# Kernel tuning notes

Measured on AMD Instinct MI355X. Metric: run time of the kernel, lower is better.

## Reference

```python
import jax, jax.numpy as jnp
import numpy as np

B, L, TQ, D, H, S = 4, 64, 8, 768, 12, 2000
E = D // H
EPS = 1e-5


def _ln(x, g, b):
    m = jnp.mean(x, axis=-1, keepdims=True)
    v = jnp.mean(jnp.square(x - m), axis=-1, keepdims=True)
    return (x - m) * jax.lax.rsqrt(v + EPS) * g + b


def setup_inputs() -> dict:
    key = jax.random.key(0)
    ks = jax.random.split(key, 8)
    w = 0.02
    return {
        "target_tokens": jax.random.normal(ks[0], (B, L, TQ, D), jnp.float32),
        "key_bank": jax.random.normal(ks[1], (S, D), jnp.float32),
        "value_bank": jax.random.normal(ks[2], (S, D), jnp.float32),
        "bank_mask": jnp.ones((S,), jnp.int32),
        "Wq": jax.random.normal(ks[3], (D, D), jnp.float32) * w,
        "bq": jnp.zeros((D,), jnp.float32),
        "Wk": jax.random.normal(ks[4], (D, D), jnp.float32) * w,
        "bk": jnp.zeros((D,), jnp.float32),
        "Wv": jax.random.normal(ks[5], (D, D), jnp.float32) * w,
        "bv": jnp.zeros((D,), jnp.float32),
        "Wo": jax.random.normal(ks[6], (D, D), jnp.float32) * w,
        "bo": jnp.zeros((D,), jnp.float32),
        "g_q": jnp.ones((D,), jnp.float32),
        "beta_q": jnp.zeros((D,), jnp.float32),
        "g_kv": jnp.ones((D,), jnp.float32),
        "beta_kv": jnp.zeros((D,), jnp.float32),
    }


def reference(target_tokens, key_bank, value_bank, bank_mask,
              Wq, bq, Wk, bk, Wv, bv, Wo, bo,
              g_q, beta_q, g_kv, beta_kv):
    scale = 1.0 / np.sqrt(E)
    # LayerNorms
    Q_in = _ln(target_tokens, g_q, beta_q)            # (B,L,Tq,D)
    K_in = _ln(key_bank, g_kv, beta_kv)               # (S,D)
    V_in = _ln(value_bank, g_kv, beta_kv)             # (S,D)
    # Projections (torch Linear: x @ W.T + b)
    Q = (jnp.einsum('bltd,ed->blte', Q_in, Wq) + bq).reshape(B, L, TQ, H, E)
    K = (jnp.einsum('sd,ed->se', K_in, Wk) + bk).reshape(S, H, E)
    V = (jnp.einsum('sd,ed->se', V_in, Wv) + bv).reshape(S, H, E)
    # Scores over the bank (bank is shared across batch)
    scores = jnp.einsum('blthe,she->bhlts', Q, K) * scale  # (B,H,L,Tq,S)
    mask = bank_mask[None, None, None, None, :] != 0
    scores = jnp.where(mask, scores, -jnp.inf)
    A = jax.nn.softmax(scores, axis=-1)
    out = jnp.einsum('bhlts,she->blthe', A, V)             # (B,L,Tq,H,E)
    out_pooled = out.mean(axis=2).reshape(B, L, H * E)     # pool='mean' over Tq
    y = jnp.einsum('bld,ed->ble', out_pooled, Wo) + bo     # (B,L,D)
    return y
```

## Files before the change

kernel.cpp:

```cpp
#include <hip/hip_runtime.h>
#include <stdint.h>

typedef unsigned short u16;
typedef float f32x4 __attribute__((ext_vector_type(4)));
typedef __bf16 bf16x8 __attribute__((ext_vector_type(8)));

#define DDIM 768
#define NHEAD 12
#define EDIM 64
#define SREAL 2000
#define SPAD 2048
#define NQ 2048
#define NSPLIT 4

__device__ __forceinline__ u16 f2bf(float f) {
    unsigned u = __float_as_uint(f);
    return (u16)((u + 0x7fffu + ((u >> 16) & 1u)) >> 16);
}
__device__ __forceinline__ float bf2f(u16 v) {
    return __uint_as_float(((unsigned)v) << 16);
}

__device__ __forceinline__ void async16(const void* g, void* l) {
    __builtin_amdgcn_global_load_lds(
        (const __attribute__((address_space(1))) void*)(const void*)g,
        (__attribute__((address_space(3))) void*)l, 16, 0, 0);
}

__global__ __launch_bounds__(256) void prep_kernel(
    const float* __restrict__ Wq, const float* __restrict__ Wk, const float* __restrict__ Wv,
    const float* __restrict__ Wo,
    u16* __restrict__ Wqb, u16* __restrict__ Wkb, u16* __restrict__ Wvb, u16* __restrict__ Wob,
    const float* __restrict__ tgt, const float* __restrict__ keyb, const float* __restrict__ valb,
    const float* __restrict__ g_q, const float* __restrict__ b_q,
    const float* __restrict__ g_kv, const float* __restrict__ b_kv,
    u16* __restrict__ lnQ, u16* __restrict__ lnK, u16* __restrict__ lnV)
{
    int bx = blockIdx.x;
    if (bx < 2304) {
        int g = bx * 256 + threadIdx.x;
        const float* src; u16* dst; int idx; float sc = 1.f;
        if (g < 147456)      { src = Wq; dst = Wqb; idx = g; sc = 0.125f; }
        else if (g < 294912) { src = Wk; dst = Wkb; idx = g - 147456; }
        else if (g < 442368) { src = Wv; dst = Wvb; idx = g - 294912; }
        else                 { src = Wo; dst = Wob; idx = g - 442368; }
        f32x4 a = ((const f32x4*)src)[idx];
        ushort4 o;
        o.x = f2bf(a[0] * sc); o.y = f2bf(a[1] * sc);
        o.z = f2bf(a[2] * sc); o.w = f2bf(a[3] * sc);
        ((ushort4*)dst)[idx] = o;
        return;
    }
    int row = (bx - 2304) * 4 + (threadIdx.x >> 6);
    int l = threadIdx.x & 63;
    const float* src = nullptr; const float* gg; const float* bb; u16* dst;
    bool zero = false;
    if (row < 2048) {
        src = tgt + (size_t)row * DDIM; gg = g_q; bb = b_q; dst = lnQ + (size_t)row * DDIM;
    } else if (row < 4096) {
        int r = row - 2048; gg = g_kv; bb = b_kv; dst = lnK + (size_t)r * DDIM;
        if (r < SREAL) src = keyb + (size_t)r * DDIM; else zero = true;
    } else {
        int r = row - 4096; gg = g_kv; bb = b_kv; dst = lnV + (size_t)r * DDIM;
        if (r < SREAL) src = valb + (size_t)r * DDIM; else zero = true;
    }
    if (zero) {
        ushort4 z; z.x = 0; z.y = 0; z.z = 0; z.w = 0;
#pragma unroll
        for (int i = 0; i < 3; i++) ((ushort4*)dst)[l + 64 * i] = z;
        return;
    }
    f32x4 a[3];
#pragma unroll
    for (int i = 0; i < 3; i++) a[i] = ((const f32x4*)src)[l + 64 * i];
    float s = 0.f;
#pragma unroll
    for (int i = 0; i < 3; i++) { s += a[i][0] + a[i][1] + a[i][2] + a[i][3]; }
#pragma unroll
    for (int m = 1; m < 64; m <<= 1) s += __shfl_xor(s, m, 64);
    float mean = s * (1.f / 768.f);
    float v = 0.f;
#pragma unroll
    for (int i = 0; i < 3; i++)
#pragma unroll
        for (int j = 0; j < 4; j++) { float d = a[i][j] - mean; v += d * d; }
#pragma unroll
    for (int m = 1; m < 64; m <<= 1) v += __shfl_xor(v, m, 64);
    float rstd = rsqrtf(v * (1.f / 768.f) + 1e-5f);
#pragma unroll
    for (int i = 0; i < 3; i++) {
        f32x4 g4 = ((const f32x4*)gg)[l + 64 * i];
        f32x4 b4 = ((const f32x4*)bb)[l + 64 * i];
        ushort4 o;
        o.x = f2bf((a[i][0] - mean) * rstd * g4[0] + b4[0]);
        o.y = f2bf((a[i][1] - mean) * rstd * g4[1] + b4[1]);
        o.z = f2bf((a[i][2] - mean) * rstd * g4[2] + b4[2]);
        o.w = f2bf((a[i][3] - mean) * rstd * g4[3] + b4[3]);
        ((ushort4*)dst)[l + 64 * i] = o;
    }
}

__global__ __launch_bounds__(256) void proj_kernel(
    const u16* __restrict__ lnQ, const u16* __restrict__ lnK, const u16* __restrict__ lnV,
    const u16* __restrict__ Wqb, const u16* __restrict__ Wkb, const u16* __restrict__ Wvb,
    const float* __restrict__ bq, const float* __restrict__ bk, const float* __restrict__ bv,
    u16* __restrict__ Qm, u16* __restrict__ Km, u16* __restrict__ VmT)
{
    __shared__ u16 Ash[2][128 * 64];
    __shared__ u16 Bsh[2][64 * 64];
    const u16* A; const u16* W; const float* bias; float bscale; int z = blockIdx.z;
    if (z == 0)      { A = lnQ; W = Wqb; bias = bq; bscale = 0.125f; }
    else if (z == 1) { A = lnK; W = Wkb; bias = bk; bscale = 1.f; }
    else             { A = lnV; W = Wvb; bias = bv; bscale = 1.f; }
    int n0 = blockIdx.x * 64, m0 = blockIdx.y * 128;
    int t = threadIdx.x, l = t & 63, quad = l >> 4, c16 = l & 15;
    int w = t >> 6;

    f32x4 acc[2][4];
    f32x4 zz = {0.f, 0.f, 0.f, 0.f};
#pragma unroll
    for (int mi = 0; mi < 2; mi++)
#pragma unroll
        for (int ni = 0; ni < 4; ni++) acc[mi][ni] = zz;

#pragma unroll
    for (int i = 0; i < 4; i++) {
        int ch = i * 256 + t;
        int r = ch >> 3, pc = ch & 7, jc = pc ^ (r & 7);
        async16(A + (size_t)(m0 + r) * DDIM + jc * 8, (char*)Ash[0] + ch * 16);
    }
#pragma unroll
    for (int i = 0; i < 2; i++) {
        int ch = i * 256 + t;
        int r = ch >> 3, pc = ch & 7, jc = pc ^ (r & 7);
        async16(W + (size_t)(n0 + r) * DDIM + jc * 8, (char*)Bsh[0] + ch * 16);
    }
    for (int kt = 0; kt < 12; kt++) {
        int cur = kt & 1;
        __syncthreads();
        if (kt < 11) {
            int k0 = (kt + 1) * 64;
#pragma unroll
            for (int i = 0; i < 4; i++) {
                int ch = i * 256 + t;
                int r = ch >> 3, pc = ch & 7, jc = pc ^ (r & 7);
                async16(A + (size_t)(m0 + r) * DDIM + k0 + jc * 8, (char*)Ash[cur ^ 1] + ch * 16);
            }
#pragma unroll
            for (int i = 0; i < 2; i++) {
                int ch = i * 256 + t;
                int r = ch >> 3, pc = ch & 7, jc = pc ^ (r & 7);
                async16(W + (size_t)(n0 + r) * DDIM + k0 + jc * 8, (char*)Bsh[cur ^ 1] + ch * 16);
            }
        }
#pragma unroll
        for (int kk = 0; kk < 2; kk++) {
            bf16x8 a[2], b[4];
#pragma unroll
            for (int mi = 0; mi < 2; mi++) {
                int row = w * 32 + mi * 16 + c16;
                int p = (kk * 4 + quad) ^ (row & 7);
                a[mi] = *(const bf16x8*)(Ash[cur] + row * 64 + p * 8);
            }
#pragma unroll
            for (int ni = 0; ni < 4; ni++) {
                int row = ni * 16 + c16;
                int p = (kk * 4 + quad) ^ (row & 7);
                b[ni] = *(const bf16x8*)(Bsh[cur] + row * 64 + p * 8);
            }
#pragma unroll
            for (int mi = 0; mi < 2; mi++)
#pragma unroll
                for (int ni = 0; ni < 4; ni++)
                    acc[mi][ni] = __builtin_amdgcn_mfma_f32_16x16x32_bf16(a[mi], b[ni], acc[mi][ni], 0, 0, 0);
        }
        __syncthreads();
    }
    if (z < 2) {
        u16* out = (z == 0) ? Qm : Km;
        int Mact = (z == 0) ? NQ : SREAL;
#pragma unroll
        for (int mi = 0; mi < 2; mi++)
#pragma unroll
            for (int ni = 0; ni < 4; ni++) {
                int n = n0 + ni * 16 + c16;
                float bval = bias[n] * bscale;
#pragma unroll
                for (int r = 0; r < 4; r++) {
                    int m = m0 + w * 32 + mi * 16 + quad * 4 + r;
                    float val = (m < Mact) ? (acc[mi][ni][r] + bval) : 0.f;
                    out[(size_t)m * DDIM + n] = f2bf(val);
                }
            }
    } else {
#pragma unroll
        for (int mi = 0; mi < 2; mi++)
#pragma unroll
            for (int ni = 0; ni < 4; ni++) {
                int n = n0 + ni * 16 + c16;
                float bval = bias[n];
                int mbase = m0 + w * 32 + mi * 16 + quad * 4;
                ushort4 o;
                o.x = (mbase + 0 < SREAL) ? f2bf(acc[mi][ni][0] + bval) : (u16)0;
                o.y = (mbase + 1 < SREAL) ? f2bf(acc[mi][ni][1] + bval) : (u16)0;
                o.z = (mbase + 2 < SREAL) ? f2bf(acc[mi][ni][2] + bval) : (u16)0;
                o.w = (mbase + 3 < SREAL) ? f2bf(acc[mi][ni][3] + bval) : (u16)0;
                *(ushort4*)(VmT + (size_t)n * SPAD + mbase) = o;
            }
    }
}

__global__ __launch_bounds__(256, 4) void attn_kernel(
    const u16* __restrict__ Qm, const u16* __restrict__ Km, const u16* __restrict__ VmT,
    const int* __restrict__ bank_mask,
    u16* __restrict__ Opart, float* __restrict__ Lpart)
{
    __shared__ __align__(16) u16 SH[64 * 64 * 3];
    __shared__ float mk[64];
    u16* Ksh = SH;
    u16* Vsh = SH + 4096;
    u16* Psh = SH + 8192;
    int b = blockIdx.x;
    int xcd = b & 7, j = b >> 3;
    int grp = xcd * 6 + (j >> 5);
    int qt = j & 31;
    int sp = grp / NHEAD, h = grp - sp * NHEAD;
    int q0 = qt * 64;
    int t = threadIdx.x, w = t >> 6, l = t & 63, quad = l >> 4, c16 = l & 15;

    bf16x8 qf[2];
#pragma unroll
    for (int kk = 0; kk < 2; kk++) {
        int row = q0 + w * 16 + c16;
        qf[kk] = *(const bf16x8*)(Qm + (size_t)row * DDIM + h * EDIM + kk * 32 + quad * 8);
    }
    bf16x8 ones;
#pragma unroll
    for (int i = 0; i < 8; i++) ones[i] = (__bf16)1.0f;

    f32x4 zz = {0.f, 0.f, 0.f, 0.f};
    f32x4 of[4], ol;
#pragma unroll
    for (int nei = 0; nei < 4; nei++) of[nei] = zz;
    ol = zz;

    for (int sc = 0; sc < 8; sc++) {
        int s0 = sp * 512 + sc * 64;
#pragma unroll
        for (int i = 0; i < 2; i++) {
            int ch = i * 256 + t;
            int r = ch >> 3, pc = ch & 7, jc = pc ^ (r & 7);
            async16(Km + (size_t)(s0 + r) * DDIM + h * EDIM + jc * 8, (char*)Ksh + ch * 16);
        }
#pragma unroll
        for (int i = 0; i < 2; i++) {
            int ch = i * 256 + t;
            int e = ch >> 3, pc = ch & 7, jc = pc ^ (e & 7);
            async16(VmT + (size_t)(h * EDIM + e) * SPAD + s0 + jc * 8, (char*)Vsh + ch * 16);
        }
        if (t < 64) {
            int s = s0 + t;
            mk[t] = (s < SREAL && bank_mask[s] != 0) ? 1.f : 0.f;
        }
        __syncthreads();

        f32x4 sacc[4];
#pragma unroll
        for (int ni = 0; ni < 4; ni++) sacc[ni] = zz;
#pragma unroll
        for (int kk = 0; kk < 2; kk++) {
            bf16x8 kb[4];
#pragma unroll
            for (int ni = 0; ni < 4; ni++) {
                int row = ni * 16 + c16;
                int p = (kk * 4 + quad) ^ (row & 7);
                kb[ni] = *(const bf16x8*)(Ksh + row * 64 + p * 8);
            }
#pragma unroll
            for (int ni = 0; ni < 4; ni++)
                sacc[ni] = __builtin_amdgcn_mfma_f32_16x16x32_bf16(qf[kk], kb[ni], sacc[ni], 0, 0, 0);
        }
        float m01[4];
#pragma unroll
        for (int ni = 0; ni < 4; ni++) m01[ni] = mk[ni * 16 + c16];
#pragma unroll
        for (int ni = 0; ni < 4; ni++)
#pragma unroll
            for (int r = 0; r < 4; r++)
                sacc[ni][r] = __expf(sacc[ni][r]) * m01[ni];

#pragma unroll
        for (int ni = 0; ni < 4; ni++)
#pragma unroll
            for (int r = 0; r < 4; r++) {
                int row = w * 16 + quad * 4 + r;
                int col = ni * 16 + c16;
                int p = (col >> 3) ^ (row & 7);
                Psh[row * 64 + p * 8 + (col & 7)] = f2bf(sacc[ni][r]);
            }

#pragma unroll
        for (int kk = 0; kk < 2; kk++) {
            bf16x8 pa, vb[4];
            {
                int row = w * 16 + c16;
                int p = (kk * 4 + quad) ^ (row & 7);
                pa = *(const bf16x8*)(Psh + row * 64 + p * 8);
            }
#pragma unroll
            for (int nei = 0; nei < 4; nei++) {
                int e = nei * 16 + c16;
                int p = (kk * 4 + quad) ^ (e & 7);
                vb[nei] = *(const bf16x8*)(Vsh + e * 64 + p * 8);
            }
#pragma unroll
            for (int nei = 0; nei < 4; nei++)
                of[nei] = __builtin_amdgcn_mfma_f32_16x16x32_bf16(pa, vb[nei], of[nei], 0, 0, 0);
            ol = __builtin_amdgcn_mfma_f32_16x16x32_bf16(pa, ones, ol, 0, 0, 0);
        }
        __syncthreads();
    }

    float* Ost = (float*)SH + w * (16 * 68);
#pragma unroll
    for (int nei = 0; nei < 4; nei++)
#pragma unroll
        for (int r = 0; r < 4; r++)
            Ost[(quad * 4 + r) * 68 + nei * 16 + c16] = of[nei][r];
    int qq = l >> 2, cc = (l & 3) ^ (qq & 3);
    int base = grp * 32 + qt;
    uint4 packed[2];
    u16* pk = (u16*)packed;
#pragma unroll
    for (int jj = 0; jj < 4; jj++) {
        f32x4 v = *(const f32x4*)(Ost + qq * 68 + cc * 16 + jj * 4);
        pk[jj * 4 + 0] = f2bf(v[0]); pk[jj * 4 + 1] = f2bf(v[1]);
        pk[jj * 4 + 2] = f2bf(v[2]); pk[jj * 4 + 3] = f2bf(v[3]);
    }
    {
        u16* dst = Opart + (size_t)base * 4096 + (w * 16 + qq) * 64 + cc * 16;
        *(uint4*)dst = packed[0];
        *(uint4*)(dst + 8) = packed[1];
    }
    if (c16 == 0) {
#pragma unroll
        for (int r = 0; r < 4; r++) {
            int rin = w * 16 + quad * 4 + r;
            Lpart[(size_t)base * 64 + rin] = ol[r];
        }
    }
}

__global__ __launch_bounds__(256) void combine_kernel(
    const u16* __restrict__ Opart, const float* __restrict__ Lpart,
    u16* __restrict__ pooledb)
{
    int gi = blockIdx.x * 4 + (threadIdx.x >> 6);
    int e = threadIdx.x & 63;
    int lq = gi / NHEAD, h = gi - lq * NHEAD;
    float acc = 0.f;
#pragma unroll
    for (int row = 0; row < 8; row++) {
        int qrow = lq * 8 + row;
        int qt = qrow >> 6, rin = qrow & 63;
        float Ls = 0.f, val = 0.f;
#pragma unroll
        for (int sp = 0; sp < NSPLIT; sp++) {
            int base = (sp * NHEAD + h) * 32 + qt;
            Ls += Lpart[(size_t)base * 64 + rin];
            val += bf2f(Opart[(size_t)base * 4096 + rin * 64 + e]);
        }
        acc += val / Ls;
    }
    pooledb[(size_t)lq * DDIM + h * EDIM + e] = f2bf(acc * 0.125f);
}

__global__ __launch_bounds__(256) void wo_kernel(
    const u16* __restrict__ pb, const u16* __restrict__ Wob,
    const float* __restrict__ bo, float* __restrict__ y)
{
    __shared__ u16 Ash[64 * 128];
    __shared__ u16 Bsh[64 * 128];
    int m0 = blockIdx.x * 64, n0 = blockIdx.y * 64;
    int t = threadIdx.x, w = t >> 6, l = t & 63, quad = l >> 4, c16 = l & 15;

    f32x4 acc[4];
    f32x4 zz = {0.f, 0.f, 0.f, 0.f};
#pragma unroll
    for (int ni = 0; ni < 4; ni++) acc[ni] = zz;

    for (int kt = 0; kt < 6; kt++) {
        int k0 = kt * 128;
#pragma unroll
        for (int i = 0; i < 4; i++) {
            int ch = i * 256 + t;
            int r = ch >> 4, pc = ch & 15, jc = pc ^ (r & 15);
            async16(pb + (size_t)(m0 + r) * DDIM + k0 + jc * 8, (char*)Ash + ch * 16);
            async16(Wob + (size_t)(n0 + r) * DDIM + k0 + jc * 8, (char*)Bsh + ch * 16);
        }
        __syncthreads();
#pragma unroll
        for (int kk = 0; kk < 4; kk++) {
            int p = (kk * 4 + quad) ^ c16;
            bf16x8 a = *(const bf16x8*)(Ash + (w * 16 + c16) * 128 + p * 8);
            bf16x8 b[4];
#pragma unroll
            for (int ni = 0; ni < 4; ni++)
                b[ni] = *(const bf16x8*)(Bsh + (ni * 16 + c16) * 128 + p * 8);
#pragma unroll
            for (int ni = 0; ni < 4; ni++)
                acc[ni] = __builtin_amdgcn_mfma_f32_16x16x32_bf16(a, b[ni], acc[ni], 0, 0, 0);
        }
        __syncthreads();
    }
#pragma unroll
    for (int ni = 0; ni < 4; ni++) {
        int n = n0 + ni * 16 + c16;
        float bval = bo[n];
#pragma unroll
        for (int r = 0; r < 4; r++) {
            int m = m0 + w * 16 + quad * 4 + r;
            y[(size_t)m * DDIM + n] = acc[ni][r] + bval;
        }
    }
}

extern "C" void kernel_launch(void* const* d_in, const int* in_sizes, int n_in,
                              void* d_out, int out_size, void* d_ws, size_t ws_size,
                              hipStream_t stream)
{
    const float* tgt     = (const float*)d_in[0];
    const float* keyb    = (const float*)d_in[1];
    const float* valb    = (const float*)d_in[2];
    const int*   mask    = (const int*)d_in[3];
    const float* Wq      = (const float*)d_in[4];
    const float* bq      = (const float*)d_in[5];
    const float* Wk      = (const float*)d_in[6];
    const float* bk      = (const float*)d_in[7];
    const float* Wv      = (const float*)d_in[8];
    const float* bv      = (const float*)d_in[9];
    const float* Wo      = (const float*)d_in[10];
    const float* bo      = (const float*)d_in[11];
    const float* g_q     = (const float*)d_in[12];
    const float* beta_q  = (const float*)d_in[13];
    const float* g_kv    = (const float*)d_in[14];
    const float* beta_kv = (const float*)d_in[15];
    float* y = (float*)d_out;

    char* ws = (char*)d_ws;
    u16* Qm  = (u16*)(ws + 0);
    u16* Km  = (u16*)(ws + 3145728);
    u16* VmT = (u16*)(ws + 6291456);
    u16* Wob = (u16*)(ws + 9437184);
    u16* lnQ = (u16*)(ws + 10616832);
    u16* lnK = (u16*)(ws + 13762560);
    u16* lnV = (u16*)(ws + 16908288);
    u16* Wqb = (u16*)(ws + 20054016);
    u16* Wkb = (u16*)(ws + 21233664);
    u16* Wvb = (u16*)(ws + 22413312);
    u16*   Opart   = (u16*)(ws + 10616832);
    float* Lpart   = (float*)(ws + 23592960);
    u16*   pooledb = (u16*)(ws + 23986176);

    hipLaunchKernelGGL(prep_kernel, dim3(3840), dim3(256), 0, stream,
                       Wq, Wk, Wv, Wo, Wqb, Wkb, Wvb, Wob,
                       tgt, keyb, valb, g_q, beta_q, g_kv, beta_kv, lnQ, lnK, lnV);
    hipLaunchKernelGGL(proj_kernel, dim3(12, 16, 3), dim3(256), 0, stream,
                       lnQ, lnK, lnV, Wqb, Wkb, Wvb, bq, bk, bv, Qm, Km, VmT);
    hipLaunchKernelGGL(attn_kernel, dim3(1536), dim3(256), 0, stream,
                       Qm, Km, VmT, mask, Opart, Lpart);
    hipLaunchKernelGGL(combine_kernel, dim3(768), dim3(256), 0, stream,
                       Opart, Lpart, pooledb);
    hipLaunchKernelGGL(wo_kernel, dim3(4, 12), dim3(256), 0, stream,
                       pooledb, Wob, bo, y);
}
```

Baseline: 159.3 us.

## Double-buffer K/V tiles, double query rows per attention block, vectorize combine

The attention kernel now handles 128 query rows per block (two 16-row MFMA tiles per wave), so each K/V tile loaded into LDS is reused across twice as many queries and the grid halves. K/V chunks are double-buffered, with the next chunk prefetched asynchronously while the current one is computed, which removes one barrier per iteration. The combine kernel reads packed 8-element vectors and reduces across rows with shuffles. In exchange, register and LDS use go up and occupancy drops from 4 to 3 blocks per launch bound, and with only 768 blocks the load balance is coarser.

```diff
diff --git a/kernel.cpp b/kernel.cpp
--- a/kernel.cpp
+++ b/kernel.cpp
@@ -210,63 +210,86 @@
     }
 }
 
-__global__ __launch_bounds__(256, 4) void attn_kernel(
+__global__ __launch_bounds__(256, 3) void attn_kernel(
     const u16* __restrict__ Qm, const u16* __restrict__ Km, const u16* __restrict__ VmT,
     const int* __restrict__ bank_mask,
     u16* __restrict__ Opart, float* __restrict__ Lpart)
 {
-    __shared__ __align__(16) u16 SH[64 * 64 * 3];
-    __shared__ float mk[64];
-    u16* Ksh = SH;
-    u16* Vsh = SH + 4096;
-    u16* Psh = SH + 8192;
+    __shared__ __align__(16) u16 SH[24576];
+    __shared__ float mk[2][64];
+    u16* Kb = SH;
+    u16* Vb = SH + 8192;
+    u16* Psh = SH + 16384;
     int b = blockIdx.x;
     int xcd = b & 7, j = b >> 3;
-    int grp = xcd * 6 + (j >> 5);
-    int qt = j & 31;
+    int grp = xcd * 6 + (j >> 4);
+    int qt = j & 15;
     int sp = grp / NHEAD, h = grp - sp * NHEAD;
-    int q0 = qt * 64;
+    int q0 = qt * 128, s00 = sp * 512;
     int t = threadIdx.x, w = t >> 6, l = t & 63, quad = l >> 4, c16 = l & 15;
 
-    bf16x8 qf[2];
-#pragma unroll
-    for (int kk = 0; kk < 2; kk++) {
-        int row = q0 + w * 16 + c16;
-        qf[kk] = *(const bf16x8*)(Qm + (size_t)row * DDIM + h * EDIM + kk * 32 + quad * 8);
-    }
+    bf16x8 qf[2][2];
+#pragma unroll
+    for (int mi = 0; mi < 2; mi++)
+#pragma unroll
+        for (int kk = 0; kk < 2; kk++) {
+            int row = q0 + w * 32 + mi * 16 + c16;
+            qf[mi][kk] = *(const bf16x8*)(Qm + (size_t)row * DDIM + h * EDIM + kk * 32 + quad * 8);
+        }
     bf16x8 ones;
 #pragma unroll
     for (int i = 0; i < 8; i++) ones[i] = (__bf16)1.0f;
 
     f32x4 zz = {0.f, 0.f, 0.f, 0.f};
-    f32x4 of[4], ol;
-#pragma unroll
-    for (int nei = 0; nei < 4; nei++) of[nei] = zz;
-    ol = zz;
+    f32x4 of[2][4], ol[2];
+#pragma unroll
+    for (int mi = 0; mi < 2; mi++) {
+#pragma unroll
+        for (int nei = 0; nei < 4; nei++) of[mi][nei] = zz;
+        ol[mi] = zz;
+    }
+
+    {
+        int ch0 = t, ch1 = 256 + t;
+        int r0 = ch0 >> 3, jc0 = (ch0 & 7) ^ (r0 & 7);
+        int r1 = ch1 >> 3, jc1 = (ch1 & 7) ^ (r1 & 7);
+        async16(Km + (size_t)(s00 + r0) * DDIM + h * EDIM + jc0 * 8, (char*)Kb + ch0 * 16);
+        async16(Km + (size_t)(s00 + r1) * DDIM + h * EDIM + jc1 * 8, (char*)Kb + ch1 * 16);
+        async16(VmT + (size_t)(h * EDIM + r0) * SPAD + s00 + jc0 * 8, (char*)Vb + ch0 * 16);
+        async16(VmT + (size_t)(h * EDIM + r1) * SPAD + s00 + jc1 * 8, (char*)Vb + ch1 * 16);
+        if (t < 64) {
+            int s = s00 + t;
+            mk[0][t] = (s < SREAL && bank_mask[s] != 0) ? 1.f : 0.f;
+        }
+    }
 
     for (int sc = 0; sc < 8; sc++) {
-        int s0 = sp * 512 + sc * 64;
-#pragma unroll
-        for (int i = 0; i < 2; i++) {
-            int ch = i * 256 + t;
-            int r = ch >> 3, pc = ch & 7, jc = pc ^ (r & 7);
-            async16(Km + (size_t)(s0 + r) * DDIM + h * EDIM + jc * 8, (char*)Ksh + ch * 16);
-        }
-#pragma unroll
-        for (int i = 0; i < 2; i++) {
-            int ch = i * 256 + t;
-            int e = ch >> 3, pc = ch & 7, jc = pc ^ (e & 7);
-            async16(VmT + (size_t)(h * EDIM + e) * SPAD + s0 + jc * 8, (char*)Vsh + ch * 16);
-        }
-        if (t < 64) {
-            int s = s0 + t;
-            mk[t] = (s < SREAL && bank_mask[s] != 0) ? 1.f : 0.f;
-        }
+        int cur = sc & 1;
         __syncthreads();
-
-        f32x4 sacc[4];
-#pragma unroll
-        for (int ni = 0; ni < 4; ni++) sacc[ni] = zz;
+        if (sc < 7) {
+            int s0n = s00 + (sc + 1) * 64;
+            char* Kd = (char*)Kb + (cur ^ 1) * 8192;
+            char* Vd = (char*)Vb + (cur ^ 1) * 8192;
+            int ch0 = t, ch1 = 256 + t;
+            int r0 = ch0 >> 3, jc0 = (ch0 & 7) ^ (r0 & 7);
+            int r1 = ch1 >> 3, jc1 = (ch1 & 7) ^ (r1 & 7);
+            async16(Km + (size_t)(s0n + r0) * DDIM + h * EDIM + jc0 * 8, Kd + ch0 * 16);
+            async16(Km + (size_t)(s0n + r1) * DDIM + h * EDIM + jc1 * 8, Kd + ch1 * 16);
+            async16(VmT + (size_t)(h * EDIM + r0) * SPAD + s0n + jc0 * 8, Vd + ch0 * 16);
+            async16(VmT + (size_t)(h * EDIM + r1) * SPAD + s0n + jc1 * 8, Vd + ch1 * 16);
+            if (t < 64) {
+                int s = s0n + t;
+                mk[cur ^ 1][t] = (s < SREAL && bank_mask[s] != 0) ? 1.f : 0.f;
+            }
+        }
+        const u16* Ksh = Kb + cur * 4096;
+        const u16* Vsh = Vb + cur * 4096;
+
+        f32x4 sacc[2][4];
+#pragma unroll
+        for (int mi = 0; mi < 2; mi++)
+#pragma unroll
+            for (int ni = 0; ni < 4; ni++) sacc[mi][ni] = zz;
 #pragma unroll
         for (int kk = 0; kk < 2; kk++) {
             bf16x8 kb[4];
@@ -277,35 +300,42 @@
                 kb[ni] = *(const bf16x8*)(Ksh + row * 64 + p * 8);
             }
 #pragma unroll
+            for (int mi = 0; mi < 2; mi++)
+#pragma unroll
+                for (int ni = 0; ni < 4; ni++)
+                    sacc[mi][ni] = __builtin_amdgcn_mfma_f32_16x16x32_bf16(qf[mi][kk], kb[ni], sacc[mi][ni], 0, 0, 0);
+        }
+        float m01[4];
+#pragma unroll
+        for (int ni = 0; ni < 4; ni++) m01[ni] = mk[cur][ni * 16 + c16];
+#pragma unroll
+        for (int mi = 0; mi < 2; mi++)
+#pragma unroll
             for (int ni = 0; ni < 4; ni++)
-                sacc[ni] = __builtin_amdgcn_mfma_f32_16x16x32_bf16(qf[kk], kb[ni], sacc[ni], 0, 0, 0);
-        }
-        float m01[4];
-#pragma unroll
-        for (int ni = 0; ni < 4; ni++) m01[ni] = mk[ni * 16 + c16];
-#pragma unroll
-        for (int ni = 0; ni < 4; ni++)
-#pragma unroll
-            for (int r = 0; r < 4; r++)
-                sacc[ni][r] = __expf(sacc[ni][r]) * m01[ni];
-
-#pragma unroll
-        for (int ni = 0; ni < 4; ni++)
-#pragma unroll
-            for (int r = 0; r < 4; r++) {
-                int row = w * 16 + quad * 4 + r;
-                int col = ni * 16 + c16;
-                int p = (col >> 3) ^ (row & 7);
-                Psh[row * 64 + p * 8 + (col & 7)] = f2bf(sacc[ni][r]);
-            }
+#pragma unroll
+                for (int r = 0; r < 4; r++)
+                    sacc[mi][ni][r] = __expf(sacc[mi][ni][r]) * m01[ni];
+
+#pragma unroll
+        for (int mi = 0; mi < 2; mi++)
+#pragma unroll
+            for (int ni = 0; ni < 4; ni++)
+#pragma unroll
+                for (int r = 0; r < 4; r++) {
+                    int row = w * 32 + mi * 16 + quad * 4 + r;
+                    int col = ni * 16 + c16;
+                    int p = (col >> 3) ^ (row & 7);
+                    Psh[row * 64 + p * 8 + (col & 7)] = f2bf(sacc[mi][ni][r]);
+                }
 
 #pragma unroll
         for (int kk = 0; kk < 2; kk++) {
-            bf16x8 pa, vb[4];
-            {
-                int row = w * 16 + c16;
+            bf16x8 pa[2], vb[4];
+#pragma unroll
+            for (int mi = 0; mi < 2; mi++) {
+                int row = w * 32 + mi * 16 + c16;
                 int p = (kk * 4 + quad) ^ (row & 7);
-                pa = *(const bf16x8*)(Psh + row * 64 + p * 8);
+                pa[mi] = *(const bf16x8*)(Psh + row * 64 + p * 8);
             }
 #pragma unroll
             for (int nei = 0; nei < 4; nei++) {
@@ -314,40 +344,46 @@
                 vb[nei] = *(const bf16x8*)(Vsh + e * 64 + p * 8);
             }
 #pragma unroll
-            for (int nei = 0; nei < 4; nei++)
-                of[nei] = __builtin_amdgcn_mfma_f32_16x16x32_bf16(pa, vb[nei], of[nei], 0, 0, 0);
-            ol = __builtin_amdgcn_mfma_f32_16x16x32_bf16(pa, ones, ol, 0, 0, 0);
-        }
-        __syncthreads();
-    }
+            for (int mi = 0; mi < 2; mi++) {
+#pragma unroll
+                for (int nei = 0; nei < 4; nei++)
+                    of[mi][nei] = __builtin_amdgcn_mfma_f32_16x16x32_bf16(pa[mi], vb[nei], of[mi][nei], 0, 0, 0);
+                ol[mi] = __builtin_amdgcn_mfma_f32_16x16x32_bf16(pa[mi], ones, ol[mi], 0, 0, 0);
+            }
+        }
+    }
+    __syncthreads();
 
     float* Ost = (float*)SH + w * (16 * 68);
-#pragma unroll
-    for (int nei = 0; nei < 4; nei++)
-#pragma unroll
-        for (int r = 0; r < 4; r++)
-            Ost[(quad * 4 + r) * 68 + nei * 16 + c16] = of[nei][r];
     int qq = l >> 2, cc = (l & 3) ^ (qq & 3);
-    int base = grp * 32 + qt;
-    uint4 packed[2];
-    u16* pk = (u16*)packed;
-#pragma unroll
-    for (int jj = 0; jj < 4; jj++) {
-        f32x4 v = *(const f32x4*)(Ost + qq * 68 + cc * 16 + jj * 4);
-        pk[jj * 4 + 0] = f2bf(v[0]); pk[jj * 4 + 1] = f2bf(v[1]);
-        pk[jj * 4 + 2] = f2bf(v[2]); pk[jj * 4 + 3] = f2bf(v[3]);
-    }
-    {
-        u16* dst = Opart + (size_t)base * 4096 + (w * 16 + qq) * 64 + cc * 16;
+    int base = grp * 16 + qt;
+#pragma unroll
+    for (int mi = 0; mi < 2; mi++) {
+#pragma unroll
+        for (int nei = 0; nei < 4; nei++)
+#pragma unroll
+            for (int r = 0; r < 4; r++)
+                Ost[(quad * 4 + r) * 68 + nei * 16 + c16] = of[mi][nei][r];
+        uint4 packed[2];
+        u16* pk = (u16*)packed;
+#pragma unroll
+        for (int jj = 0; jj < 4; jj++) {
+            f32x4 v = *(const f32x4*)(Ost + qq * 68 + cc * 16 + jj * 4);
+            pk[jj * 4 + 0] = f2bf(v[0]); pk[jj * 4 + 1] = f2bf(v[1]);
+            pk[jj * 4 + 2] = f2bf(v[2]); pk[jj * 4 + 3] = f2bf(v[3]);
+        }
+        u16* dst = Opart + (size_t)base * 8192 + (w * 32 + mi * 16 + qq) * 64 + cc * 16;
         *(uint4*)dst = packed[0];
         *(uint4*)(dst + 8) = packed[1];
     }
     if (c16 == 0) {
 #pragma unroll
-        for (int r = 0; r < 4; r++) {
-            int rin = w * 16 + quad * 4 + r;
-            Lpart[(size_t)base * 64 + rin] = ol[r];
-        }
+        for (int mi = 0; mi < 2; mi++)
+#pragma unroll
+            for (int r = 0; r < 4; r++) {
+                int rin = w * 32 + mi * 16 + quad * 4 + r;
+                Lpart[(size_t)base * 128 + rin] = ol[mi][r];
+            }
     }
 }
 
@@ -356,23 +392,39 @@
     u16* __restrict__ pooledb)
 {
     int gi = blockIdx.x * 4 + (threadIdx.x >> 6);
-    int e = threadIdx.x & 63;
+    int l = threadIdx.x & 63;
     int lq = gi / NHEAD, h = gi - lq * NHEAD;
-    float acc = 0.f;
-#pragma unroll
-    for (int row = 0; row < 8; row++) {
-        int qrow = lq * 8 + row;
-        int qt = qrow >> 6, rin = qrow & 63;
-        float Ls = 0.f, val = 0.f;
-#pragma unroll
-        for (int sp = 0; sp < NSPLIT; sp++) {
-            int base = (sp * NHEAD + h) * 32 + qt;
-            Ls += Lpart[(size_t)base * 64 + rin];
-            val += bf2f(Opart[(size_t)base * 4096 + rin * 64 + e]);
-        }
-        acc += val / Ls;
-    }
-    pooledb[(size_t)lq * DDIM + h * EDIM + e] = f2bf(acc * 0.125f);
+    int rs = l >> 3, oct = l & 7;
+    int qrow = lq * 8 + rs;
+    int qt = qrow >> 7, rin = qrow & 127;
+    float vsum[8];
+#pragma unroll
+    for (int j = 0; j < 8; j++) vsum[j] = 0.f;
+    float Lsum = 0.f;
+#pragma unroll
+    for (int sp = 0; sp < NSPLIT; sp++) {
+        int base = (sp * NHEAD + h) * 16 + qt;
+        uint4 pk = *(const uint4*)(Opart + (size_t)base * 8192 + rin * 64 + oct * 8);
+        const u16* pu = (const u16*)&pk;
+#pragma unroll
+        for (int j = 0; j < 8; j++) vsum[j] += bf2f(pu[j]);
+        Lsum += Lpart[(size_t)base * 128 + rin];
+    }
+    float inv = 1.f / Lsum;
+    float c[8];
+#pragma unroll
+    for (int j = 0; j < 8; j++) c[j] = vsum[j] * inv;
+#pragma unroll
+    for (int mm = 8; mm < 64; mm <<= 1)
+#pragma unroll
+        for (int j = 0; j < 8; j++) c[j] += __shfl_xor(c[j], mm, 64);
+    if (rs == 0) {
+        uint4 packed;
+        u16* pk = (u16*)&packed;
+#pragma unroll
+        for (int j = 0; j < 8; j++) pk[j] = f2bf(c[j] * 0.125f);
+        *(uint4*)(pooledb + (size_t)lq * DDIM + h * EDIM + oct * 8) = packed;
+    }
 }
 
 __global__ __launch_bounds__(256) void wo_kernel(
@@ -467,7 +519,7 @@
                        tgt, keyb, valb, g_q, beta_q, g_kv, beta_kv, lnQ, lnK, lnV);
     hipLaunchKernelGGL(proj_kernel, dim3(12, 16, 3), dim3(256), 0, stream,
                        lnQ, lnK, lnV, Wqb, Wkb, Wvb, bq, bk, bv, Qm, Km, VmT);
-    hipLaunchKernelGGL(attn_kernel, dim3(1536), dim3(256), 0, stream,
+    hipLaunchKernelGGL(attn_kernel, dim3(768), dim3(256), 0, stream,
                        Qm, Km, VmT, mask, Opart, Lpart);
     hipLaunchKernelGGL(combine_kernel, dim3(768), dim3(256), 0, stream,
                        Opart, Lpart, pooledb);
```

Measured after the change: 161.8 us. About the same (+1.5%).
